# Performance work log

Measured on AMD Instinct MI355X. Metric: run time of the kernel, lower is better.

Reference implementation:

```python
import jax, jax.numpy as jnp
import numpy as np

VOCAB = 8192
DIM = 256
COMMITMENT = 0.25


def setup_inputs() -> dict:
    key = jax.random.key(0)
    kx, ke = jax.random.split(key)
    x = jax.random.normal(kx, (8, 4096, DIM), dtype=jnp.float32)
    # torch init: uniform(-1/vocab_size, 1/vocab_size)
    emb = jax.random.uniform(ke, (VOCAB, DIM), dtype=jnp.float32,
                             minval=-1.0 / VOCAB, maxval=1.0 / VOCAB)
    return {"x": x, "emb": emb}


def reference(x, emb):
    x2 = jnp.sum(x * x, axis=-1, keepdims=True)          # [B, N, 1]
    e2 = jnp.sum(emb * emb, axis=-1)                      # [V]
    d2 = x2 + e2 - 2.0 * jnp.einsum('bnd,vd->bnv', x, emb)  # [B, N, V]
    idx = jnp.argmin(d2, axis=-1)                         # [B, N]
    quantised = emb[idx]                                  # [B, N, D]

    codebook_loss = jnp.mean((quantised - jax.lax.stop_gradient(x)) ** 2)
    e_latent_loss = jnp.mean((jax.lax.stop_gradient(quantised) - x) ** 2)
    loss = codebook_loss + COMMITMENT * e_latent_loss

    quantised_st = x + jax.lax.stop_gradient(quantised - x)  # straight-through
    return quantised_st, loss, codebook_loss, idx
```

## Files before the change

kernel.cpp:

```cpp
#include <hip/hip_runtime.h>

#define VOCAB 8192
#define DIM   256
#define NTOK  32768

#define LOSS_OFF 8388608
#define CB_OFF   8388609
#define IDX_OFF  8388610

#define X2_F     0
#define E2_F     32768
#define ACC_F    40960
#define OVF_I    40961
#define BEST_B   196608
#define EMB16_B  458752
#define SMAX_B   4718592
#define SCNT_B   38273024
#define BIN_B    38404096
#define CAP_S    8192
#define PSUM_B   46792704
#define WS_NEED  (PSUM_B + 8192 * 4)

#define M2 1.5e-4f
#define LCAP 16000

typedef __attribute__((ext_vector_type(8)))  short bf16x8;
typedef __attribute__((ext_vector_type(16))) float f32x16;

__global__ __launch_bounds__(256) void k_sums(const float* __restrict__ x,
                                              const float* __restrict__ emb,
                                              float* __restrict__ ws,
                                              unsigned long long* __restrict__ best,
                                              int* __restrict__ scnt,
                                              unsigned* __restrict__ e16u,
                                              int full) {
    const int lane = threadIdx.x & 63;
    const int wave = threadIdx.x >> 6;
    const int row  = blockIdx.x * 16 + wave * 4 + (lane >> 4);
    const int sub  = lane & 15;
    const int k    = sub & 7;
    const int half = sub >> 3;
    const float* src = (row < NTOK ? x + (size_t)row * DIM
                                   : emb + (size_t)(row - NTOK) * DIM)
                       + half * 128 + k;
    float r;
    {
        float v0 = src[0];
        float t0 = v0 * v0;
        asm volatile("" : "+v"(t0));
        r = t0;
        for (int i = 1; i < 16; ++i) {
            float w = src[8 * i];
            float u = w * w;
            asm volatile("" : "+v"(u));
            r = r + u;
        }
    }
    float t;
    t = __shfl_xor(r, 1, 64); r = r + t;
    t = __shfl_xor(r, 2, 64); r = r + t;
    t = __shfl_xor(r, 4, 64); r = r + t;
    t = __shfl_xor(r, 8, 64); r = r + t;
    if (sub == 0) ws[row] = r;

    if (full && row >= NTOK) {
        const float* er = emb + (size_t)(row - NTOK) * DIM + sub * 16;
        unsigned* op = e16u + (size_t)(row - NTOK) * 128 + sub * 8;
#pragma unroll
        for (int q = 0; q < 4; ++q) {
            const float4 f = *(const float4*)(er + q * 4);
            uint2 o;
            o.x = (__float_as_uint(f.y) & 0xFFFF0000u) | (__float_as_uint(f.x) >> 16);
            o.y = (__float_as_uint(f.w) & 0xFFFF0000u) | (__float_as_uint(f.z) >> 16);
            *(uint2*)(op + q * 2) = o;
        }
    }

    const int gid = blockIdx.x * 256 + threadIdx.x;
    if (gid == 0) {
        ws[ACC_F] = 0.0f;
        ((int*)ws)[OVF_I] = 0;
    }
    if (full) {
        if (gid < NTOK) best[gid] = ~0ULL;
        if (gid < 256)  scnt[gid] = 0;
    }
}

#define AS1 __attribute__((address_space(1)))
#define AS3 __attribute__((address_space(3)))

#define STAGE4(BUFI, N, P) do {                                                \
    const char* _src = (const char*)embh + ((size_t)(N) << 16);                \
    char* _dst = ebuf[BUFI];                                                   \
    _Pragma("unroll")                                                          \
    for (int _r = (P) * 4; _r < (P) * 4 + 4; ++_r) {                           \
        const unsigned _o = (unsigned)tid * 16u + (unsigned)_r * 8192u;        \
        __builtin_amdgcn_global_load_lds(                                      \
            (const AS1 void*)(_src + so8[_r]),                                 \
            (AS3 void*)(_dst + _o), 16, 0, 0);                                 \
    }                                                                          \
} while (0)

__device__ __forceinline__ unsigned f_ord(float v) {
    unsigned u = __float_as_uint(v);
    return u ^ ((unsigned)((int)u >> 31) | 0x80000000u);
}
__device__ __forceinline__ float f_unord(unsigned k) {
    unsigned m = (k >> 31) ? 0x80000000u : 0xFFFFFFFFu;
    return __uint_as_float(k ^ m);
}

__global__ __launch_bounds__(512, 2) void k_coarse(
        const float* __restrict__ x, const unsigned short* __restrict__ embh,
        float* __restrict__ smax,
        unsigned* __restrict__ binned, int* __restrict__ scnt,
        int* __restrict__ ovf) {
    __shared__ char ebuf[2][65536];
    __shared__ unsigned tmax[128];
    __shared__ float tthr[128];

    const int tid  = threadIdx.x;
    const int lane = tid & 63, wid = tid >> 6;
    const int g = wid & 1, csub = wid >> 1;
    const int t_wave = blockIdx.x * 128 + g * 64;

    unsigned so8[8];
#pragma unroll
    for (int r = 0; r < 8; ++r) {
        const unsigned o = (unsigned)tid * 16u + (unsigned)r * 8192u;
        so8[r] = (o & ~511u) | ((o & 511u) ^ (((o >> 9) & 31u) << 4));
    }

    bf16x8 bx[2][16];
    {
        const int tok0 = t_wave + (lane & 31);
#pragma unroll
        for (int grp = 0; grp < 2; ++grp) {
            const float* xr = x + (size_t)(tok0 + grp * 32) * DIM + (lane >> 5) * 8;
#pragma unroll
            for (int kt = 0; kt < 16; ++kt) {
                float4 f0 = *(const float4*)(xr + kt * 16);
                float4 f1 = *(const float4*)(xr + kt * 16 + 4);
                union { bf16x8 v; unsigned u[4]; } P;
                P.u[0] = (__float_as_uint(f0.y) & 0xFFFF0000u) | (__float_as_uint(f0.x) >> 16);
                P.u[1] = (__float_as_uint(f0.w) & 0xFFFF0000u) | (__float_as_uint(f0.z) >> 16);
                P.u[2] = (__float_as_uint(f1.y) & 0xFFFF0000u) | (__float_as_uint(f1.x) >> 16);
                P.u[3] = (__float_as_uint(f1.w) & 0xFFFF0000u) | (__float_as_uint(f1.z) >> 16);
                bx[grp][kt] = P.v;
            }
        }
    }

    const unsigned rl    = (unsigned)(csub * 32 + (lane & 31));
    const unsigned abase = rl * 512u + (unsigned)((lane >> 5) * 16);
    const unsigned sw    = (rl & 31u) << 4;

    STAGE4(0, 0, 0);
    STAGE4(0, 0, 1);
    asm volatile("s_waitcnt vmcnt(0)" ::: "memory");
    __builtin_amdgcn_s_barrier();

    float rmax = -3.0e38f;
    for (int n = 0; n < 64; ++n) {
        const char* cb = ebuf[n & 1];
        const int   nb = (n + 1) & 1;
        const bool  more = (n + 1 < 64);

        f32x16 acc0, acc1;
#pragma unroll
        for (int q = 0; q < 16; ++q) { acc0[q] = 0.0f; acc1[q] = 0.0f; }

#pragma unroll
        for (int p = 0; p < 4; ++p) {
            bf16x8 a0 = *(const bf16x8*)(cb + ((abase + (unsigned)(p * 4 + 0) * 32u) ^ sw));
            bf16x8 a1 = *(const bf16x8*)(cb + ((abase + (unsigned)(p * 4 + 1) * 32u) ^ sw));
            bf16x8 a2 = *(const bf16x8*)(cb + ((abase + (unsigned)(p * 4 + 2) * 32u) ^ sw));
            bf16x8 a3 = *(const bf16x8*)(cb + ((abase + (unsigned)(p * 4 + 3) * 32u) ^ sw));
            if (more && p < 2) STAGE4(nb, n + 1, p);
            __builtin_amdgcn_s_barrier();
            __builtin_amdgcn_s_setprio(1);
            acc0 = __builtin_amdgcn_mfma_f32_32x32x16_bf16(a0, bx[0][p * 4 + 0], acc0, 0, 0, 0);
            acc1 = __builtin_amdgcn_mfma_f32_32x32x16_bf16(a0, bx[1][p * 4 + 0], acc1, 0, 0, 0);
            acc0 = __builtin_amdgcn_mfma_f32_32x32x16_bf16(a1, bx[0][p * 4 + 1], acc0, 0, 0, 0);
            acc1 = __builtin_amdgcn_mfma_f32_32x32x16_bf16(a1, bx[1][p * 4 + 1], acc1, 0, 0, 0);
            acc0 = __builtin_amdgcn_mfma_f32_32x32x16_bf16(a2, bx[0][p * 4 + 2], acc0, 0, 0, 0);
            acc1 = __builtin_amdgcn_mfma_f32_32x32x16_bf16(a2, bx[1][p * 4 + 2], acc1, 0, 0, 0);
            acc0 = __builtin_amdgcn_mfma_f32_32x32x16_bf16(a3, bx[0][p * 4 + 3], acc0, 0, 0, 0);
            acc1 = __builtin_amdgcn_mfma_f32_32x32x16_bf16(a3, bx[1][p * 4 + 3], acc1, 0, 0, 0);
            __builtin_amdgcn_s_setprio(0);
            __builtin_amdgcn_s_barrier();
        }

        float m0, m1;
        {
            float a = fmaxf(fmaxf(acc0[0], acc0[1]),  fmaxf(acc0[2], acc0[3]));
            float b = fmaxf(fmaxf(acc0[4], acc0[5]),  fmaxf(acc0[6], acc0[7]));
            float c = fmaxf(fmaxf(acc0[8], acc0[9]),  fmaxf(acc0[10], acc0[11]));
            float d = fmaxf(fmaxf(acc0[12], acc0[13]),fmaxf(acc0[14], acc0[15]));
            m0 = fmaxf(fmaxf(a, b), fmaxf(c, d));
            a = fmaxf(fmaxf(acc1[0], acc1[1]),  fmaxf(acc1[2], acc1[3]));
            b = fmaxf(fmaxf(acc1[4], acc1[5]),  fmaxf(acc1[6], acc1[7]));
            c = fmaxf(fmaxf(acc1[8], acc1[9]),  fmaxf(acc1[10], acc1[11]));
            d = fmaxf(fmaxf(acc1[12], acc1[13]),fmaxf(acc1[14], acc1[15]));
            m1 = fmaxf(fmaxf(a, b), fmaxf(c, d));
        }
        m0 = fmaxf(m0, __shfl_xor(m0, 32, 64));
        m1 = fmaxf(m1, __shfl_xor(m1, 32, 64));
        const float mv = (lane < 32) ? m0 : m1;
        rmax = fmaxf(rmax, mv);
        smax[(size_t)(n * 4 + csub) * NTOK + t_wave + lane] = mv;

        if (more) asm volatile("s_waitcnt vmcnt(1)" ::: "memory");
        else      asm volatile("s_waitcnt vmcnt(0)" ::: "memory");
        __builtin_amdgcn_s_barrier();
    }

    unsigned* lbuf  = (unsigned*)ebuf;
    unsigned* lcnt  = lbuf + 2 + LCAP;
    unsigned* lbase = lcnt + 256;
    unsigned* lcur  = lbase + 256;
    if (tid < 128) tmax[tid] = 0u;
    if (tid == 0) lbuf[0] = 0u;
    if (tid < 256) { lcnt[tid] = 0u; lcur[tid] = 0u; }
    __syncthreads();
    atomicMax(&tmax[g * 64 + lane], f_ord(rmax));
    __syncthreads();
    if (tid < 128) tthr[tid] = f_unord(tmax[tid]) - M2;
    __syncthreads();

    const int t0b = blockIdx.x * 128;
    for (int r = 0; r < 64; ++r) {
        const int cell  = r * 512 + tid;
        const int stile = cell >> 7, tl = cell & 127;
        const float v = smax[(size_t)stile * NTOK + t0b + tl];
        if (v >= tthr[tl]) {
            const unsigned p = atomicAdd(&lbuf[0], 1u);
            if (p < LCAP)
                lbuf[2 + p] = ((unsigned)(t0b + tl) << 8) | (unsigned)stile;
        }
    }
    __syncthreads();
    unsigned bc = lbuf[0];
    if (bc > LCAP) { bc = LCAP; if (tid == 0) *ovf = 1; }

    for (unsigned i = tid; i < bc; i += 512)
        atomicAdd(&lcnt[lbuf[2 + i] & 255u], 1u);
    __syncthreads();
    if (tid < 256 && lcnt[tid]) {
        const unsigned b = (unsigned)atomicAdd(&scnt[tid], (int)lcnt[tid]);
        lbase[tid] = b;
        if (b + lcnt[tid] > CAP_S) *ovf = 1;
    }
    __syncthreads();
    for (unsigned i = tid; i < bc; i += 512) {
        const unsigned e = lbuf[2 + i];
        const unsigned s = e & 255u;
        const unsigned p = lbase[s] + atomicAdd(&lcur[s], 1u);
        if (p < CAP_S) binned[(size_t)s * CAP_S + p] = e;
    }
}

__device__ __forceinline__ float exact_score(const float* __restrict__ xr,
                                             const float* __restrict__ er,
                                             float x2t, float e2v) {
    float dot = 0.0f;
#pragma unroll 16
    for (int d = 0; d < DIM; d += 4) {
        const float4 e4 = *(const float4*)(er + d);
        const float4 x4 = *(const float4*)(xr + d);
        dot = fmaf(e4.x, x4.x, dot);
        dot = fmaf(e4.y, x4.y, dot);
        dot = fmaf(e4.z, x4.z, dot);
        dot = fmaf(e4.w, x4.w, dot);
    }
    const float A = x2t + e2v;
    return A - 2.0f * dot;
}

__global__ __launch_bounds__(256) void k_exact2(
        const float* __restrict__ x, const float* __restrict__ emb,
        const float* __restrict__ x2, const float* __restrict__ e2,
        const unsigned* __restrict__ binned, const int* __restrict__ scnt,
        const int* __restrict__ ovf, unsigned long long* __restrict__ best) {
    __shared__ float elds[32][257];
    __shared__ float e2s[32];
    const int s = blockIdx.x >> 3, sub = blockIdx.x & 7;
    {
        const int r = threadIdx.x >> 3, c0 = (threadIdx.x & 7) * 32;
        const float* er = emb + (size_t)(s * 32 + r) * DIM + c0;
#pragma unroll
        for (int q = 0; q < 8; ++q) {
            const float4 f = *(const float4*)(er + q * 4);
            elds[r][c0 + q * 4 + 0] = f.x; elds[r][c0 + q * 4 + 1] = f.y;
            elds[r][c0 + q * 4 + 2] = f.z; elds[r][c0 + q * 4 + 3] = f.w;
        }
        if (threadIdx.x < 32) e2s[threadIdx.x] = e2[s * 32 + threadIdx.x];
    }
    __syncthreads();

    const int lane = threadIdx.x & 63, wave = threadIdx.x >> 6;
    const int l5 = lane & 31, half = lane >> 5;
    int count = scnt[s]; if (count > CAP_S) count = CAP_S;
    const unsigned* bucket = binned + (size_t)s * CAP_S;
    const float e2v = e2s[l5];

    for (int k = (sub * 4 + wave) * 2 + half; k < count; k += 64) {
        const unsigned e = bucket[k];
        const int token  = (int)(e >> 8);
        const float* xr  = x + (size_t)token * DIM;
        const float x2t  = x2[token];
        float dot = 0.0f;
#pragma unroll 16
        for (int d = 0; d < DIM; d += 4) {
            const float4 x4 = *(const float4*)(xr + d);
            dot = fmaf(elds[l5][d + 0], x4.x, dot);
            dot = fmaf(elds[l5][d + 1], x4.y, dot);
            dot = fmaf(elds[l5][d + 2], x4.z, dot);
            dot = fmaf(elds[l5][d + 3], x4.w, dot);
        }
        const float A  = x2t + e2v;
        const float sc = A - 2.0f * dot;
        unsigned long long pk =
            ((unsigned long long)__float_as_uint(sc) << 32) | (unsigned)(s * 32 + l5);
#pragma unroll
        for (int m = 1; m < 32; m <<= 1) {
            unsigned long long o = __shfl_xor(pk, m, 64);
            if (o < pk) pk = o;
        }
        if (l5 == 0) atomicMin(&best[token], pk);
    }

    if (*ovf) {
        const size_t stride = (size_t)2048 * 256;
        for (size_t c = blockIdx.x * 256 + threadIdx.x;
             c < (size_t)NTOK * VOCAB; c += stride) {
            const int token = (int)(c >> 13);
            const int v     = (int)(c & (VOCAB - 1));
            const float sc = exact_score(x + (size_t)token * DIM, emb + (size_t)v * DIM,
                                         x2[token], e2[v]);
            unsigned long long pk =
                ((unsigned long long)__float_as_uint(sc) << 32) | (unsigned)v;
            atomicMin(&best[token], pk);
        }
    }
}

__global__ __launch_bounds__(512) void k_main_fb(
        const float* __restrict__ x, const float* __restrict__ emb,
        const float* __restrict__ x2, const float* __restrict__ e2,
        float* __restrict__ idxf) {
    __shared__ float xT[32][132];
    __shared__ float eT[32][260];
    const int tid = threadIdx.x;
    const int tx = tid & 31, ty = tid >> 5;
    const int t0 = blockIdx.x * 128;
    float x2r[8];
#pragma unroll
    for (int ii = 0; ii < 8; ++ii)
        x2r[ii] = x2[t0 + ((ii & 4) << 4) + ty * 4 + (ii & 3)];
    float tb[8]; int ti[8];
#pragma unroll
    for (int s = 0; s < 8; ++s) { tb[s] = 3.0e38f; ti[s] = 0; }
    const int xt = tid & 127, xc = tid >> 7;
    const int ev = tid & 255, ec0 = tid >> 8;
    for (int v0 = 0; v0 < VOCAB; v0 += 256) {
        float a[8][8];
#pragma unroll
        for (int i = 0; i < 8; ++i)
#pragma unroll
            for (int j = 0; j < 8; ++j) a[i][j] = 0.0f;
        for (int kk = 0; kk < DIM; kk += 32) {
            __syncthreads();
#pragma unroll
            for (int h = 0; h < 2; ++h) {
                const int kc = h * 16 + xc * 4;
                const float4 vx = *(const float4*)&x[(size_t)(t0 + xt) * DIM + kk + kc];
                xT[kc + 0][xt] = vx.x; xT[kc + 1][xt] = vx.y;
                xT[kc + 2][xt] = vx.z; xT[kc + 3][xt] = vx.w;
            }
#pragma unroll
            for (int h = 0; h < 4; ++h) {
                const int kc = (ec0 + 2 * h) * 4;
                const float4 ve = *(const float4*)&emb[(size_t)(v0 + ev) * DIM + kk + kc];
                eT[kc + 0][ev] = ve.x; eT[kc + 1][ev] = ve.y;
                eT[kc + 2][ev] = ve.z; eT[kc + 3][ev] = ve.w;
            }
            __syncthreads();
#pragma unroll 4
            for (int k = 0; k < 32; ++k) {
                float xa[8], eb[8];
                *(float4*)&xa[0] = *(const float4*)&xT[k][ty * 4];
                *(float4*)&xa[4] = *(const float4*)&xT[k][64 + ty * 4];
                *(float4*)&eb[0] = *(const float4*)&eT[k][tx * 4];
                *(float4*)&eb[4] = *(const float4*)&eT[k][128 + tx * 4];
#pragma unroll
                for (int i = 0; i < 8; ++i)
#pragma unroll
                    for (int j = 0; j < 8; ++j)
                        a[i][j] = fmaf(xa[i], eb[j], a[i][j]);
            }
        }
#pragma unroll
        for (int jj = 0; jj < 8; ++jj) {
            const int v = v0 + ((jj & 4) << 5) + tx * 4 + (jj & 3);
            const float evv = e2[v];
#pragma unroll
            for (int ii = 0; ii < 8; ++ii) {
                const float A  = x2r[ii] + evv;
                const float sc = A - 2.0f * a[ii][jj];
                if (sc < tb[ii]) { tb[ii] = sc; ti[ii] = v; }
            }
        }
    }
#pragma unroll
    for (int ii = 0; ii < 8; ++ii) {
        float b = tb[ii]; int bi = ti[ii];
#pragma unroll
        for (int m = 1; m < 32; m <<= 1) {
            const float ob = __shfl_xor(b, m, 64);
            const int   oi = __shfl_xor(bi, m, 64);
            if (ob < b || (ob == b && oi < bi)) { b = ob; bi = oi; }
        }
        if (tx == 0) {
            const int token = t0 + ((ii & 4) << 4) + ty * 4 + (ii & 3);
            idxf[token] = (float)bi;
        }
    }
}

__global__ __launch_bounds__(256) void k_gather(
        const float* __restrict__ x, const float* __restrict__ emb,
        const unsigned long long* __restrict__ best,
        float* __restrict__ out, float* __restrict__ psum,
        float* __restrict__ acc, int full) {
    const int token = blockIdx.x * 4 + (threadIdx.x >> 6);
    const int lane  = threadIdx.x & 63;
    float* idxf = out + IDX_OFF;
    int v;
    if (full) {
        v = (int)(unsigned)(best[token] & 0xFFFFFFFFULL);
        if (lane == 0) idxf[token] = (float)v;
    } else {
        v = (int)idxf[token];
    }
    const float4 e4 = *(const float4*)&emb[(size_t)v * DIM + lane * 4];
    const float4 x4 = *(const float4*)&x[(size_t)token * DIM + lane * 4];
    *(float4*)&out[(size_t)token * DIM + lane * 4] = e4;
    const float dx = e4.x - x4.x, dy = e4.y - x4.y, dz = e4.z - x4.z, dw = e4.w - x4.w;
    float s = dx*dx + dy*dy + dz*dz + dw*dw;
#pragma unroll
    for (int m = 1; m < 64; m <<= 1) s += __shfl_xor(s, m, 64);
    __shared__ float wsum[4];
    if (lane == 0) wsum[threadIdx.x >> 6] = s;
    __syncthreads();
    if (threadIdx.x == 0) {
        const float bsum = wsum[0] + wsum[1] + wsum[2] + wsum[3];
        if (full) psum[blockIdx.x] = bsum;
        else      atomicAdd(acc, bsum);
    }
}

__global__ __launch_bounds__(256) void k_final(const float* __restrict__ psum,
                                               const float* __restrict__ acc,
                                               float* __restrict__ out, int full) {
    float s = 0.0f;
    if (full) {
        for (int i = threadIdx.x; i < 8192; i += 256) s += psum[i];
#pragma unroll
        for (int m = 1; m < 64; m <<= 1) s += __shfl_xor(s, m, 64);
        __shared__ float wsum[4];
        if ((threadIdx.x & 63) == 0) wsum[threadIdx.x >> 6] = s;
        __syncthreads();
        s = wsum[0] + wsum[1] + wsum[2] + wsum[3];
    } else {
        s = *acc;
    }
    if (threadIdx.x == 0) {
        const float cb = s * (1.0f / 8388608.0f);
        out[LOSS_OFF] = 1.25f * cb;
        out[CB_OFF]   = cb;
    }
}

extern "C" void kernel_launch(void* const* d_in, const int* in_sizes, int n_in,
                              void* d_out, int out_size, void* d_ws, size_t ws_size,
                              hipStream_t stream) {
    const float* x   = (const float*)d_in[0];
    const float* emb = (const float*)d_in[1];
    float* out  = (float*)d_out;
    char*  wsB  = (char*)d_ws;
    float* wsF  = (float*)d_ws;

    float* x2   = wsF + X2_F;
    float* e2   = wsF + E2_F;
    float* acc  = wsF + ACC_F;
    int*   ovf  = (int*)wsF + OVF_I;
    unsigned long long* best = (unsigned long long*)(wsB + BEST_B);
    unsigned short*     e16  = (unsigned short*)(wsB + EMB16_B);
    float*              smax = (float*)(wsB + SMAX_B);
    int*                scnt = (int*)(wsB + SCNT_B);
    unsigned*           binned = (unsigned*)(wsB + BIN_B);
    float*              psum = (float*)(wsB + PSUM_B);
    float* idxf = out + IDX_OFF;

    const int full = (ws_size >= (size_t)WS_NEED) ? 1 : 0;

    k_sums<<<(NTOK + VOCAB) / 16, 256, 0, stream>>>(x, emb, wsF, best, scnt,
                                                    (unsigned*)e16, full);
    if (full) {
        k_coarse<<<256, 512, 0, stream>>>(x, e16, smax, binned, scnt, ovf);
        k_exact2<<<2048, 256, 0, stream>>>(x, emb, x2, e2, binned, scnt, ovf, best);
    } else {
        k_main_fb<<<NTOK / 128, 512, 0, stream>>>(x, emb, x2, e2, idxf);
    }
    k_gather<<<NTOK / 4, 256, 0, stream>>>(x, emb, best, out, psum, acc, full);
    k_final <<<1, 256, 0, stream>>>(psum, acc, out, full);
}
```

Measured before the change: 285.4 us.

## Shrink coarse-pass tiles to 64 tokens per block with single-stage prefetch

The coarse bf16 MFMA scan is retiled from 128 tokens and 512 threads per block to 64 tokens and 256 threads. Each block now stages 32KB codebook chunks of 64 codes, issuing the whole next-chunk prefetch at the start of each iteration and dropping the per-quarter barriers. The intent is to cut LDS use and sync overhead, launch twice as many blocks for better occupancy, and halve register pressure from one accumulator per wave. In exchange, each codebook tile is reused across only half as many tokens, which doubles L2 traffic for the codebook, and the local candidate buffer cap is lowered.

Measured after the change: 311.8 us. 9.3% more time.

```diff
diff --git a/kernel.cpp b/kernel.cpp
--- a/kernel.cpp
+++ b/kernel.cpp
@@ -22,7 +22,7 @@
 #define WS_NEED  (PSUM_B + 8192 * 4)
 
 #define M2 1.5e-4f
-#define LCAP 16000
+#define LCAP 8192
 
 typedef __attribute__((ext_vector_type(8)))  short bf16x8;
 typedef __attribute__((ext_vector_type(16))) float f32x16;
@@ -90,12 +90,12 @@
 #define AS1 __attribute__((address_space(1)))
 #define AS3 __attribute__((address_space(3)))
 
-#define STAGE4(BUFI, N, P) do {                                                \
-    const char* _src = (const char*)embh + ((size_t)(N) << 16);                \
+#define STAGE8(BUFI, N) do {                                                   \
+    const char* _src = (const char*)embh + ((size_t)(N) << 15);                \
     char* _dst = ebuf[BUFI];                                                   \
     _Pragma("unroll")                                                          \
-    for (int _r = (P) * 4; _r < (P) * 4 + 4; ++_r) {                           \
-        const unsigned _o = (unsigned)tid * 16u + (unsigned)_r * 8192u;        \
+    for (int _r = 0; _r < 8; ++_r) {                                           \
+        const unsigned _o = (unsigned)tid * 16u + (unsigned)_r * 4096u;        \
         __builtin_amdgcn_global_load_lds(                                      \
             (const AS1 void*)(_src + so8[_r]),                                 \
             (AS3 void*)(_dst + _o), 16, 0, 0);                                 \
@@ -111,44 +111,41 @@
     return __uint_as_float(k ^ m);
 }
 
-__global__ __launch_bounds__(512, 2) void k_coarse(
+__global__ __launch_bounds__(256, 2) void k_coarse(
         const float* __restrict__ x, const unsigned short* __restrict__ embh,
         float* __restrict__ smax,
         unsigned* __restrict__ binned, int* __restrict__ scnt,
         int* __restrict__ ovf) {
-    __shared__ char ebuf[2][65536];
-    __shared__ unsigned tmax[128];
-    __shared__ float tthr[128];
+    __shared__ char ebuf[2][32768];
+    __shared__ unsigned tmax[64];
+    __shared__ float tthr[64];
 
     const int tid  = threadIdx.x;
     const int lane = tid & 63, wid = tid >> 6;
     const int g = wid & 1, csub = wid >> 1;
-    const int t_wave = blockIdx.x * 128 + g * 64;
+    const int t_blk = blockIdx.x * 64;
 
     unsigned so8[8];
 #pragma unroll
     for (int r = 0; r < 8; ++r) {
-        const unsigned o = (unsigned)tid * 16u + (unsigned)r * 8192u;
+        const unsigned o = (unsigned)tid * 16u + (unsigned)r * 4096u;
         so8[r] = (o & ~511u) | ((o & 511u) ^ (((o >> 9) & 31u) << 4));
     }
 
-    bf16x8 bx[2][16];
+    bf16x8 bx[16];
     {
-        const int tok0 = t_wave + (lane & 31);
-#pragma unroll
-        for (int grp = 0; grp < 2; ++grp) {
-            const float* xr = x + (size_t)(tok0 + grp * 32) * DIM + (lane >> 5) * 8;
-#pragma unroll
-            for (int kt = 0; kt < 16; ++kt) {
-                float4 f0 = *(const float4*)(xr + kt * 16);
-                float4 f1 = *(const float4*)(xr + kt * 16 + 4);
-                union { bf16x8 v; unsigned u[4]; } P;
-                P.u[0] = (__float_as_uint(f0.y) & 0xFFFF0000u) | (__float_as_uint(f0.x) >> 16);
-                P.u[1] = (__float_as_uint(f0.w) & 0xFFFF0000u) | (__float_as_uint(f0.z) >> 16);
-                P.u[2] = (__float_as_uint(f1.y) & 0xFFFF0000u) | (__float_as_uint(f1.x) >> 16);
-                P.u[3] = (__float_as_uint(f1.w) & 0xFFFF0000u) | (__float_as_uint(f1.z) >> 16);
-                bx[grp][kt] = P.v;
-            }
+        const float* xr = x + (size_t)(t_blk + g * 32 + (lane & 31)) * DIM
+                            + (lane >> 5) * 8;
+#pragma unroll
+        for (int kt = 0; kt < 16; ++kt) {
+            float4 f0 = *(const float4*)(xr + kt * 16);
+            float4 f1 = *(const float4*)(xr + kt * 16 + 4);
+            union { bf16x8 v; unsigned u[4]; } P;
+            P.u[0] = (__float_as_uint(f0.y) & 0xFFFF0000u) | (__float_as_uint(f0.x) >> 16);
+            P.u[1] = (__float_as_uint(f0.w) & 0xFFFF0000u) | (__float_as_uint(f0.z) >> 16);
+            P.u[2] = (__float_as_uint(f1.y) & 0xFFFF0000u) | (__float_as_uint(f1.x) >> 16);
+            P.u[3] = (__float_as_uint(f1.w) & 0xFFFF0000u) | (__float_as_uint(f1.z) >> 16);
+            bx[kt] = P.v;
         }
     }
 
@@ -156,60 +153,46 @@
     const unsigned abase = rl * 512u + (unsigned)((lane >> 5) * 16);
     const unsigned sw    = (rl & 31u) << 4;
 
-    STAGE4(0, 0, 0);
-    STAGE4(0, 0, 1);
+    STAGE8(0, 0);
     asm volatile("s_waitcnt vmcnt(0)" ::: "memory");
     __builtin_amdgcn_s_barrier();
 
     float rmax = -3.0e38f;
-    for (int n = 0; n < 64; ++n) {
+    for (int n = 0; n < 128; ++n) {
         const char* cb = ebuf[n & 1];
-        const int   nb = (n + 1) & 1;
-        const bool  more = (n + 1 < 64);
-
-        f32x16 acc0, acc1;
-#pragma unroll
-        for (int q = 0; q < 16; ++q) { acc0[q] = 0.0f; acc1[q] = 0.0f; }
-
-#pragma unroll
-        for (int p = 0; p < 4; ++p) {
-            bf16x8 a0 = *(const bf16x8*)(cb + ((abase + (unsigned)(p * 4 + 0) * 32u) ^ sw));
-            bf16x8 a1 = *(const bf16x8*)(cb + ((abase + (unsigned)(p * 4 + 1) * 32u) ^ sw));
-            bf16x8 a2 = *(const bf16x8*)(cb + ((abase + (unsigned)(p * 4 + 2) * 32u) ^ sw));
-            bf16x8 a3 = *(const bf16x8*)(cb + ((abase + (unsigned)(p * 4 + 3) * 32u) ^ sw));
-            if (more && p < 2) STAGE4(nb, n + 1, p);
-            __builtin_amdgcn_s_barrier();
+        const bool  more = (n + 1 < 128);
+        if (more) STAGE8((n + 1) & 1, n + 1);
+
+        f32x16 acc;
+#pragma unroll
+        for (int q = 0; q < 16; ++q) acc[q] = 0.0f;
+
+#pragma unroll
+        for (int b4 = 0; b4 < 4; ++b4) {
+            bf16x8 a0 = *(const bf16x8*)(cb + ((abase + (unsigned)(b4 * 4 + 0) * 32u) ^ sw));
+            bf16x8 a1 = *(const bf16x8*)(cb + ((abase + (unsigned)(b4 * 4 + 1) * 32u) ^ sw));
+            bf16x8 a2 = *(const bf16x8*)(cb + ((abase + (unsigned)(b4 * 4 + 2) * 32u) ^ sw));
+            bf16x8 a3 = *(const bf16x8*)(cb + ((abase + (unsigned)(b4 * 4 + 3) * 32u) ^ sw));
             __builtin_amdgcn_s_setprio(1);
-            acc0 = __builtin_amdgcn_mfma_f32_32x32x16_bf16(a0, bx[0][p * 4 + 0], acc0, 0, 0, 0);
-            acc1 = __builtin_amdgcn_mfma_f32_32x32x16_bf16(a0, bx[1][p * 4 + 0], acc1, 0, 0, 0);
-            acc0 = __builtin_amdgcn_mfma_f32_32x32x16_bf16(a1, bx[0][p * 4 + 1], acc0, 0, 0, 0);
-            acc1 = __builtin_amdgcn_mfma_f32_32x32x16_bf16(a1, bx[1][p * 4 + 1], acc1, 0, 0, 0);
-            acc0 = __builtin_amdgcn_mfma_f32_32x32x16_bf16(a2, bx[0][p * 4 + 2], acc0, 0, 0, 0);
-            acc1 = __builtin_amdgcn_mfma_f32_32x32x16_bf16(a2, bx[1][p * 4 + 2], acc1, 0, 0, 0);
-            acc0 = __builtin_amdgcn_mfma_f32_32x32x16_bf16(a3, bx[0][p * 4 + 3], acc0, 0, 0, 0);
-            acc1 = __builtin_amdgcn_mfma_f32_32x32x16_bf16(a3, bx[1][p * 4 + 3], acc1, 0, 0, 0);
+            acc = __builtin_amdgcn_mfma_f32_32x32x16_bf16(a0, bx[b4 * 4 + 0], acc, 0, 0, 0);
+            acc = __builtin_amdgcn_mfma_f32_32x32x16_bf16(a1, bx[b4 * 4 + 1], acc, 0, 0, 0);
+            acc = __builtin_amdgcn_mfma_f32_32x32x16_bf16(a2, bx[b4 * 4 + 2], acc, 0, 0, 0);
+            acc = __builtin_amdgcn_mfma_f32_32x32x16_bf16(a3, bx[b4 * 4 + 3], acc, 0, 0, 0);
             __builtin_amdgcn_s_setprio(0);
-            __builtin_amdgcn_s_barrier();
-        }
-
-        float m0, m1;
+        }
+
+        float m0;
         {
-            float a = fmaxf(fmaxf(acc0[0], acc0[1]),  fmaxf(acc0[2], acc0[3]));
-            float b = fmaxf(fmaxf(acc0[4], acc0[5]),  fmaxf(acc0[6], acc0[7]));
-            float c = fmaxf(fmaxf(acc0[8], acc0[9]),  fmaxf(acc0[10], acc0[11]));
-            float d = fmaxf(fmaxf(acc0[12], acc0[13]),fmaxf(acc0[14], acc0[15]));
+            float a = fmaxf(fmaxf(acc[0], acc[1]),  fmaxf(acc[2], acc[3]));
+            float b = fmaxf(fmaxf(acc[4], acc[5]),  fmaxf(acc[6], acc[7]));
+            float c = fmaxf(fmaxf(acc[8], acc[9]),  fmaxf(acc[10], acc[11]));
+            float d = fmaxf(fmaxf(acc[12], acc[13]),fmaxf(acc[14], acc[15]));
             m0 = fmaxf(fmaxf(a, b), fmaxf(c, d));
-            a = fmaxf(fmaxf(acc1[0], acc1[1]),  fmaxf(acc1[2], acc1[3]));
-            b = fmaxf(fmaxf(acc1[4], acc1[5]),  fmaxf(acc1[6], acc1[7]));
-            c = fmaxf(fmaxf(acc1[8], acc1[9]),  fmaxf(acc1[10], acc1[11]));
-            d = fmaxf(fmaxf(acc1[12], acc1[13]),fmaxf(acc1[14], acc1[15]));
-            m1 = fmaxf(fmaxf(a, b), fmaxf(c, d));
         }
         m0 = fmaxf(m0, __shfl_xor(m0, 32, 64));
-        m1 = fmaxf(m1, __shfl_xor(m1, 32, 64));
-        const float mv = (lane < 32) ? m0 : m1;
-        rmax = fmaxf(rmax, mv);
-        smax[(size_t)(n * 4 + csub) * NTOK + t_wave + lane] = mv;
+        rmax = fmaxf(rmax, m0);
+        if (lane < 32)
+            smax[(size_t)(n * 2 + csub) * NTOK + t_blk + g * 32 + lane] = m0;
 
         if (more) asm volatile("s_waitcnt vmcnt(1)" ::: "memory");
         else      asm volatile("s_waitcnt vmcnt(0)" ::: "memory");
@@ -220,40 +203,39 @@
     unsigned* lcnt  = lbuf + 2 + LCAP;
     unsigned* lbase = lcnt + 256;
     unsigned* lcur  = lbase + 256;
-    if (tid < 128) tmax[tid] = 0u;
+    if (tid < 64) tmax[tid] = 0u;
     if (tid == 0) lbuf[0] = 0u;
-    if (tid < 256) { lcnt[tid] = 0u; lcur[tid] = 0u; }
-    __syncthreads();
-    atomicMax(&tmax[g * 64 + lane], f_ord(rmax));
-    __syncthreads();
-    if (tid < 128) tthr[tid] = f_unord(tmax[tid]) - M2;
-    __syncthreads();
-
-    const int t0b = blockIdx.x * 128;
+    { lcnt[tid] = 0u; lcur[tid] = 0u; }
+    __syncthreads();
+    if (lane < 32) atomicMax(&tmax[g * 32 + lane], f_ord(rmax));
+    __syncthreads();
+    if (tid < 64) tthr[tid] = f_unord(tmax[tid]) - M2;
+    __syncthreads();
+
     for (int r = 0; r < 64; ++r) {
-        const int cell  = r * 512 + tid;
-        const int stile = cell >> 7, tl = cell & 127;
-        const float v = smax[(size_t)stile * NTOK + t0b + tl];
+        const int cell  = r * 256 + tid;
+        const int stile = cell >> 6, tl = cell & 63;
+        const float v = smax[(size_t)stile * NTOK + t_blk + tl];
         if (v >= tthr[tl]) {
             const unsigned p = atomicAdd(&lbuf[0], 1u);
             if (p < LCAP)
-                lbuf[2 + p] = ((unsigned)(t0b + tl) << 8) | (unsigned)stile;
+                lbuf[2 + p] = ((unsigned)(t_blk + tl) << 8) | (unsigned)stile;
         }
     }
     __syncthreads();
     unsigned bc = lbuf[0];
     if (bc > LCAP) { bc = LCAP; if (tid == 0) *ovf = 1; }
 
-    for (unsigned i = tid; i < bc; i += 512)
+    for (unsigned i = tid; i < bc; i += 256)
         atomicAdd(&lcnt[lbuf[2 + i] & 255u], 1u);
     __syncthreads();
-    if (tid < 256 && lcnt[tid]) {
+    if (lcnt[tid]) {
         const unsigned b = (unsigned)atomicAdd(&scnt[tid], (int)lcnt[tid]);
         lbase[tid] = b;
         if (b + lcnt[tid] > CAP_S) *ovf = 1;
     }
     __syncthreads();
-    for (unsigned i = tid; i < bc; i += 512) {
+    for (unsigned i = tid; i < bc; i += 256) {
         const unsigned e = lbuf[2 + i];
         const unsigned s = e & 255u;
         const unsigned p = lbase[s] + atomicAdd(&lcur[s], 1u);
@@ -509,7 +491,7 @@
     k_sums<<<(NTOK + VOCAB) / 16, 256, 0, stream>>>(x, emb, wsF, best, scnt,
                                                     (unsigned*)e16, full);
     if (full) {
-        k_coarse<<<256, 512, 0, stream>>>(x, e16, smax, binned, scnt, ovf);
+        k_coarse<<<NTOK / 64, 256, 0, stream>>>(x, e16, smax, binned, scnt, ovf);
         k_exact2<<<2048, 256, 0, stream>>>(x, emb, x2, e2, binned, scnt, ovf, best);
     } else {
         k_main_fb<<<NTOK / 128, 512, 0, stream>>>(x, emb, x2, e2, idxf);
```

## Pre-swizzle bf16 codebook into MFMA fragment layout and load directly to registers

Applied to the files above, without the earlier changes.

The prep kernel now writes the bf16 codebook in a layout matching the MFMA A-operand fragments. The coarse kernel drops the LDS double-buffered staging with its barriers and instead loads fragments straight from global into registers, with software prefetch of the next tile overlapping the MFMAs. This removes LDS traffic and block-wide barriers and shrinks shared memory use, which may raise occupancy. In exchange, each wave issues its own global loads, so traffic to L2 rises, and latency hiding now rests on register double-buffering.

Result: no change. 283.9 us (median of 2 runs) (-0.5%).

```diff
diff --git a/kernel.cpp b/kernel.cpp
--- a/kernel.cpp
+++ b/kernel.cpp
@@ -64,16 +64,25 @@
     if (sub == 0) ws[row] = r;
 
     if (full && row >= NTOK) {
-        const float* er = emb + (size_t)(row - NTOK) * DIM + sub * 16;
-        unsigned* op = e16u + (size_t)(row - NTOK) * 128 + sub * 8;
-#pragma unroll
-        for (int q = 0; q < 4; ++q) {
-            const float4 f = *(const float4*)(er + q * 4);
-            uint2 o;
-            o.x = (__float_as_uint(f.y) & 0xFFFF0000u) | (__float_as_uint(f.x) >> 16);
-            o.y = (__float_as_uint(f.w) & 0xFFFF0000u) | (__float_as_uint(f.z) >> 16);
-            *(uint2*)(op + q * 2) = o;
-        }
+        const int c = row - NTOK;
+        const float* er = emb + (size_t)c * DIM + sub * 16;
+        const float4 f0 = *(const float4*)(er + 0);
+        const float4 f1 = *(const float4*)(er + 4);
+        const float4 f2 = *(const float4*)(er + 8);
+        const float4 f3 = *(const float4*)(er + 12);
+        uint4 u0, u1;
+        u0.x = (__float_as_uint(f0.y) & 0xFFFF0000u) | (__float_as_uint(f0.x) >> 16);
+        u0.y = (__float_as_uint(f0.w) & 0xFFFF0000u) | (__float_as_uint(f0.z) >> 16);
+        u0.z = (__float_as_uint(f1.y) & 0xFFFF0000u) | (__float_as_uint(f1.x) >> 16);
+        u0.w = (__float_as_uint(f1.w) & 0xFFFF0000u) | (__float_as_uint(f1.z) >> 16);
+        u1.x = (__float_as_uint(f2.y) & 0xFFFF0000u) | (__float_as_uint(f2.x) >> 16);
+        u1.y = (__float_as_uint(f2.w) & 0xFFFF0000u) | (__float_as_uint(f2.z) >> 16);
+        u1.z = (__float_as_uint(f3.y) & 0xFFFF0000u) | (__float_as_uint(f3.x) >> 16);
+        u1.w = (__float_as_uint(f3.w) & 0xFFFF0000u) | (__float_as_uint(f3.z) >> 16);
+        unsigned* dst = e16u + (((size_t)(c >> 5) * 16384 + (size_t)sub * 1024
+                               + (size_t)(c & 31) * 16) >> 2);
+        *(uint4*)dst         = u0;
+        *(uint4*)(dst + 128) = u1;
     }
 
     const int gid = blockIdx.x * 256 + threadIdx.x;
@@ -86,21 +95,6 @@
         if (gid < 256)  scnt[gid] = 0;
     }
 }
-
-#define AS1 __attribute__((address_space(1)))
-#define AS3 __attribute__((address_space(3)))
-
-#define STAGE4(BUFI, N, P) do {                                                \
-    const char* _src = (const char*)embh + ((size_t)(N) << 16);                \
-    char* _dst = ebuf[BUFI];                                                   \
-    _Pragma("unroll")                                                          \
-    for (int _r = (P) * 4; _r < (P) * 4 + 4; ++_r) {                           \
-        const unsigned _o = (unsigned)tid * 16u + (unsigned)_r * 8192u;        \
-        __builtin_amdgcn_global_load_lds(                                      \
-            (const AS1 void*)(_src + so8[_r]),                                 \
-            (AS3 void*)(_dst + _o), 16, 0, 0);                                 \
-    }                                                                          \
-} while (0)
 
 __device__ __forceinline__ unsigned f_ord(float v) {
     unsigned u = __float_as_uint(v);
@@ -116,21 +110,15 @@
         float* __restrict__ smax,
         unsigned* __restrict__ binned, int* __restrict__ scnt,
         int* __restrict__ ovf) {
-    __shared__ char ebuf[2][65536];
     __shared__ unsigned tmax[128];
     __shared__ float tthr[128];
+    __shared__ unsigned lbuf[2 + LCAP];
+    __shared__ unsigned lcnt[256], lbase[256], lcur[256];
 
     const int tid  = threadIdx.x;
     const int lane = tid & 63, wid = tid >> 6;
     const int g = wid & 1, csub = wid >> 1;
     const int t_wave = blockIdx.x * 128 + g * 64;
-
-    unsigned so8[8];
-#pragma unroll
-    for (int r = 0; r < 8; ++r) {
-        const unsigned o = (unsigned)tid * 16u + (unsigned)r * 8192u;
-        so8[r] = (o & ~511u) | ((o & 511u) ^ (((o >> 9) & 31u) << 4));
-    }
 
     bf16x8 bx[2][16];
     {
@@ -152,45 +140,47 @@
         }
     }
 
-    const unsigned rl    = (unsigned)(csub * 32 + (lane & 31));
-    const unsigned abase = rl * 512u + (unsigned)((lane >> 5) * 16);
-    const unsigned sw    = (rl & 31u) << 4;
-
-    STAGE4(0, 0, 0);
-    STAGE4(0, 0, 1);
-    asm volatile("s_waitcnt vmcnt(0)" ::: "memory");
-    __builtin_amdgcn_s_barrier();
+    const char* ep = (const char*)embh + (size_t)csub * 16384 + (size_t)lane * 16;
+
+    bf16x8 afA[8], afB[8];
+#pragma unroll
+    for (int j = 0; j < 8; ++j)
+        afA[j] = *(const bf16x8*)(ep + j * 1024);
 
     float rmax = -3.0e38f;
     for (int n = 0; n < 64; ++n) {
-        const char* cb = ebuf[n & 1];
-        const int   nb = (n + 1) & 1;
-        const bool  more = (n + 1 < 64);
+        const char* epB = ep + 8192;
+#pragma unroll
+        for (int j = 0; j < 8; ++j)
+            afB[j] = *(const bf16x8*)(epB + j * 1024);
 
         f32x16 acc0, acc1;
 #pragma unroll
         for (int q = 0; q < 16; ++q) { acc0[q] = 0.0f; acc1[q] = 0.0f; }
 
-#pragma unroll
-        for (int p = 0; p < 4; ++p) {
-            bf16x8 a0 = *(const bf16x8*)(cb + ((abase + (unsigned)(p * 4 + 0) * 32u) ^ sw));
-            bf16x8 a1 = *(const bf16x8*)(cb + ((abase + (unsigned)(p * 4 + 1) * 32u) ^ sw));
-            bf16x8 a2 = *(const bf16x8*)(cb + ((abase + (unsigned)(p * 4 + 2) * 32u) ^ sw));
-            bf16x8 a3 = *(const bf16x8*)(cb + ((abase + (unsigned)(p * 4 + 3) * 32u) ^ sw));
-            if (more && p < 2) STAGE4(nb, n + 1, p);
-            __builtin_amdgcn_s_barrier();
-            __builtin_amdgcn_s_setprio(1);
-            acc0 = __builtin_amdgcn_mfma_f32_32x32x16_bf16(a0, bx[0][p * 4 + 0], acc0, 0, 0, 0);
-            acc1 = __builtin_amdgcn_mfma_f32_32x32x16_bf16(a0, bx[1][p * 4 + 0], acc1, 0, 0, 0);
-            acc0 = __builtin_amdgcn_mfma_f32_32x32x16_bf16(a1, bx[0][p * 4 + 1], acc0, 0, 0, 0);
-            acc1 = __builtin_amdgcn_mfma_f32_32x32x16_bf16(a1, bx[1][p * 4 + 1], acc1, 0, 0, 0);
-            acc0 = __builtin_amdgcn_mfma_f32_32x32x16_bf16(a2, bx[0][p * 4 + 2], acc0, 0, 0, 0);
-            acc1 = __builtin_amdgcn_mfma_f32_32x32x16_bf16(a2, bx[1][p * 4 + 2], acc1, 0, 0, 0);
-            acc0 = __builtin_amdgcn_mfma_f32_32x32x16_bf16(a3, bx[0][p * 4 + 3], acc0, 0, 0, 0);
-            acc1 = __builtin_amdgcn_mfma_f32_32x32x16_bf16(a3, bx[1][p * 4 + 3], acc1, 0, 0, 0);
-            __builtin_amdgcn_s_setprio(0);
-            __builtin_amdgcn_s_barrier();
-        }
+        __builtin_amdgcn_s_setprio(1);
+#pragma unroll
+        for (int j = 0; j < 8; ++j) {
+            acc0 = __builtin_amdgcn_mfma_f32_32x32x16_bf16(afA[j], bx[0][j], acc0, 0, 0, 0);
+            acc1 = __builtin_amdgcn_mfma_f32_32x32x16_bf16(afA[j], bx[1][j], acc1, 0, 0, 0);
+        }
+        __builtin_amdgcn_s_setprio(0);
+
+        const char* epn = ep + 65536;
+        if (n < 63) {
+#pragma unroll
+            for (int j = 0; j < 8; ++j)
+                afA[j] = *(const bf16x8*)(epn + j * 1024);
+        }
+
+        __builtin_amdgcn_s_setprio(1);
+#pragma unroll
+        for (int j = 0; j < 8; ++j) {
+            acc0 = __builtin_amdgcn_mfma_f32_32x32x16_bf16(afB[j], bx[0][8 + j], acc0, 0, 0, 0);
+            acc1 = __builtin_amdgcn_mfma_f32_32x32x16_bf16(afB[j], bx[1][8 + j], acc1, 0, 0, 0);
+        }
+        __builtin_amdgcn_s_setprio(0);
+        ep = epn;
 
         float m0, m1;
         {
@@ -210,16 +200,8 @@
         const float mv = (lane < 32) ? m0 : m1;
         rmax = fmaxf(rmax, mv);
         smax[(size_t)(n * 4 + csub) * NTOK + t_wave + lane] = mv;
-
-        if (more) asm volatile("s_waitcnt vmcnt(1)" ::: "memory");
-        else      asm volatile("s_waitcnt vmcnt(0)" ::: "memory");
-        __builtin_amdgcn_s_barrier();
-    }
-
-    unsigned* lbuf  = (unsigned*)ebuf;
-    unsigned* lcnt  = lbuf + 2 + LCAP;
-    unsigned* lbase = lcnt + 256;
-    unsigned* lcur  = lbase + 256;
+    }
+
     if (tid < 128) tmax[tid] = 0u;
     if (tid == 0) lbuf[0] = 0u;
     if (tid < 256) { lcnt[tid] = 0u; lcur[tid] = 0u; }
```
